# Kernel tuning notes

Hardware: AMD Instinct MI355X
Metric: run time of the kernel (lower is better)

## Reference

```python
import jax, jax.numpy as jnp
import numpy as np

B, L, DM = 2, 2048, 2048
H, P, N = 32, 64, 64          # n_heads, d_head, d_state
D_INNER = H * P               # 2048
PROJ = 2 * D_INNER + 2 * H * N + H  # 8224
EPS = 1e-5


def setup_inputs() -> dict:
    key = jax.random.key(0)
    k0, k1, k2 = jax.random.split(key, 3)
    return {
        "x": jax.random.normal(k0, (B, L, DM), jnp.float32),
        "W_in": jax.random.normal(k1, (PROJ, DM), jnp.float32) * (DM ** -0.5),
        "W_out": jax.random.normal(k2, (DM, D_INNER), jnp.float32) * (D_INNER ** -0.5),
        "gamma": jnp.ones((D_INNER,), jnp.float32),
        "beta": jnp.zeros((D_INNER,), jnp.float32),
        "D": jnp.ones((H, P), jnp.float32),
    }


def reference(x, W_in, W_out, gamma, beta, D):
    Bz, Lz, _ = x.shape
    zxbca = x @ W_in.T  # [B, L, PROJ]
    x_t, z_t, b_t, c_t, a_log = jnp.split(
        zxbca, [D_INNER, 2 * D_INNER, 2 * D_INNER + H * N, 2 * D_INNER + 2 * H * N], axis=-1)
    x_t = x_t.reshape(Bz, Lz, H, P)
    b_t = b_t.reshape(Bz, Lz, H, N)
    c_t = c_t.reshape(Bz, Lz, H, N)
    decay = jnp.exp(-jnp.exp(a_log))  # [B, L, H]

    def step(states, inp):
        # states: [B, H, P, N]
        xt, bt, ct, dec = inp  # [B,H,P], [B,H,N], [B,H,N], [B,H]
        states = states * dec[:, :, None, None] + xt[..., None] * bt[:, :, None, :]
        yt = jnp.einsum('bhpn,bhn->bhp', states, ct) + xt * D
        return states, yt

    init = jnp.zeros((Bz, H, P, N), x.dtype)
    xs = (jnp.moveaxis(x_t, 1, 0), jnp.moveaxis(b_t, 1, 0),
          jnp.moveaxis(c_t, 1, 0), jnp.moveaxis(decay, 1, 0))
    _, ys = jax.lax.scan(step, init, xs)  # ys: [L, B, H, P]
    y = jnp.moveaxis(ys, 0, 1).reshape(Bz, Lz, D_INNER)
    y = y * jax.nn.silu(z_t)
    mu = y.mean(-1, keepdims=True)
    var = y.var(-1, keepdims=True)
    y = (y - mu) * jax.lax.rsqrt(var + EPS) * gamma + beta
    return y @ W_out.T
```

## Files before the change

### kernel.cpp

```cpp
#include <hip/hip_runtime.h>
#include <stdint.h>
#include <stddef.h>

#define LSEQ   2048
#define DMODEL 2048
#define NH     32
#define DINNER 2048
#define PROJ   8224
#define PROJP  8192
#define NC     16
#define CHUNK  128

typedef __attribute__((ext_vector_type(4))) float f32x4;
typedef __attribute__((ext_vector_type(8))) __bf16 bf16x8;
typedef __attribute__((ext_vector_type(8))) unsigned short u16x8;

__device__ __forceinline__ unsigned short f2bf(float f) {
  union { float f; unsigned u; } uu; uu.f = f;
  unsigned r = uu.u + 0x7FFFu + ((uu.u >> 16) & 1u);
  return (unsigned short)(r >> 16);
}
__device__ __forceinline__ float bf2f(unsigned short u) {
  union { unsigned u; float f; } x; x.u = ((unsigned)u) << 16; return x.f;
}

__device__ __forceinline__ void gl_lds16(const void* g, void* l) {
  __builtin_amdgcn_global_load_lds(
      (__attribute__((address_space(1))) const void*)g,
      (__attribute__((address_space(3))) void*)l, 16, 0, 0);
}

__global__ __launch_bounds__(256) void cvt_f32_bf16(
    const float* __restrict__ in, unsigned short* __restrict__ out, int n) {
  int i = (blockIdx.x * 256 + threadIdx.x) * 4;
  if (i + 3 < n) {
    f32x4 v = *(const f32x4*)(in + i);
    ushort4 o;
    o.x = f2bf(v[0]); o.y = f2bf(v[1]); o.z = f2bf(v[2]); o.w = f2bf(v[3]);
    *(ushort4*)(out + i) = o;
  }
}

__global__ __launch_bounds__(512, 2) void gemm256(
    const unsigned short* __restrict__ A,
    const unsigned short* __restrict__ W,
    unsigned short* __restrict__ C, const int K, const int ldc, const int ntx) {
  __shared__ uint8_t sA[2][32768];
  __shared__ uint8_t sB[2][32768];
  const int tid  = threadIdx.x;
  const int lane = tid & 63;
  const int wid  = tid >> 6;
  const int wm   = wid >> 2;
  const int wnn  = wid & 3;
  const int nwg = gridDim.x;
  const int wg0 = blockIdx.x;
  const int g   = (wg0 & 7) * (nwg >> 3) + (wg0 >> 3);
  const int grp = ntx * 4;
  const int sr  = g / grp, rem = g % grp;
  const int m0  = (sr * 4 + (rem & 3)) * 256;
  const int n0  = (rem >> 2) * 256;

  const int row0 = wid * 8 + (lane >> 3);
  const int ssrc = (lane & 7) ^ (row0 & 7);
  const unsigned short* a_base = A + (size_t)(m0 + row0) * K + ssrc * 8;
  const unsigned short* b_base = W + (size_t)(n0 + row0) * K + ssrc * 8;
  const int wb = wid * 1024;

  f32x4 acc[8][4] = {};
  const int nk = K >> 6;

#pragma unroll
  for (int j = 0; j < 4; ++j) {
    gl_lds16(a_base + (size_t)j * 64 * K, &sA[0][j * 8192 + wb]);
    gl_lds16(b_base + (size_t)j * 64 * K, &sB[0][j * 8192 + wb]);
  }
  asm volatile("s_waitcnt vmcnt(0)" ::: "memory");
  asm volatile("s_barrier" ::: "memory");

  const int ra = wm * 128 + (lane & 15);
  const int rb = wnn * 64 + (lane & 15);
  const int hq = lane >> 4;

  for (int kt = 0; kt < nk; ++kt) {
    const int cur = kt & 1;
    const int nxt = cur ^ 1;
    const unsigned short* an = a_base + (size_t)(kt + 1) * 64;
    const unsigned short* wn_ = b_base + (size_t)(kt + 1) * 64;
    bf16x8 af[8], bv01[2], bv23[2];

    {
      const int s = hq;
#pragma unroll
      for (int mi = 0; mi < 8; ++mi) {
        const int r = ra + mi * 16;
        af[mi] = *(const bf16x8*)(&sA[cur][r * 128 + ((s ^ (r & 7)) << 4)]);
      }
#pragma unroll
      for (int ni = 0; ni < 2; ++ni) {
        const int r = rb + ni * 16;
        bv01[ni] = *(const bf16x8*)(&sB[cur][r * 128 + ((s ^ (r & 7)) << 4)]);
      }
    }
    asm volatile("s_barrier" ::: "memory");
    asm volatile("s_waitcnt lgkmcnt(0)" ::: "memory");
    if (kt + 1 < nk) {
      gl_lds16(an, &sA[nxt][wb]);
      gl_lds16(an + (size_t)64 * K, &sA[nxt][8192 + wb]);
      gl_lds16(wn_, &sB[nxt][wb]);
      gl_lds16(wn_ + (size_t)64 * K, &sB[nxt][8192 + wb]);
    }
    __builtin_amdgcn_s_setprio(1);
#pragma unroll
    for (int mi = 0; mi < 8; ++mi)
#pragma unroll
      for (int ni = 0; ni < 2; ++ni)
        acc[mi][ni] = __builtin_amdgcn_mfma_f32_16x16x32_bf16(
            af[mi], bv01[ni], acc[mi][ni], 0, 0, 0);
    __builtin_amdgcn_s_setprio(0);

    {
      const int s = hq;
#pragma unroll
      for (int ni = 0; ni < 2; ++ni) {
        const int r = rb + (ni + 2) * 16;
        bv23[ni] = *(const bf16x8*)(&sB[cur][r * 128 + ((s ^ (r & 7)) << 4)]);
      }
    }
    asm volatile("s_barrier" ::: "memory");
    asm volatile("s_waitcnt lgkmcnt(0)" ::: "memory");
    if (kt + 1 < nk) {
      gl_lds16(an + (size_t)128 * K, &sA[nxt][2 * 8192 + wb]);
      gl_lds16(an + (size_t)192 * K, &sA[nxt][3 * 8192 + wb]);
      gl_lds16(wn_ + (size_t)128 * K, &sB[nxt][2 * 8192 + wb]);
      gl_lds16(wn_ + (size_t)192 * K, &sB[nxt][3 * 8192 + wb]);
    }
    __builtin_amdgcn_s_setprio(1);
#pragma unroll
    for (int mi = 0; mi < 8; ++mi)
#pragma unroll
      for (int ni = 0; ni < 2; ++ni)
        acc[mi][ni + 2] = __builtin_amdgcn_mfma_f32_16x16x32_bf16(
            af[mi], bv23[ni], acc[mi][ni + 2], 0, 0, 0);
    __builtin_amdgcn_s_setprio(0);

    {
      const int s = 4 + hq;
#pragma unroll
      for (int mi = 0; mi < 8; ++mi) {
        const int r = ra + mi * 16;
        af[mi] = *(const bf16x8*)(&sA[cur][r * 128 + ((s ^ (r & 7)) << 4)]);
      }
#pragma unroll
      for (int ni = 0; ni < 2; ++ni) {
        const int r = rb + ni * 16;
        bv01[ni] = *(const bf16x8*)(&sB[cur][r * 128 + ((s ^ (r & 7)) << 4)]);
      }
    }
    asm volatile("s_barrier" ::: "memory");
    asm volatile("s_waitcnt lgkmcnt(0)" ::: "memory");
    __builtin_amdgcn_s_setprio(1);
#pragma unroll
    for (int mi = 0; mi < 8; ++mi)
#pragma unroll
      for (int ni = 0; ni < 2; ++ni)
        acc[mi][ni] = __builtin_amdgcn_mfma_f32_16x16x32_bf16(
            af[mi], bv01[ni], acc[mi][ni], 0, 0, 0);
    __builtin_amdgcn_s_setprio(0);

    {
      const int s = 4 + hq;
#pragma unroll
      for (int ni = 0; ni < 2; ++ni) {
        const int r = rb + (ni + 2) * 16;
        bv23[ni] = *(const bf16x8*)(&sB[cur][r * 128 + ((s ^ (r & 7)) << 4)]);
      }
    }
    asm volatile("s_waitcnt vmcnt(0)" ::: "memory");
    asm volatile("s_barrier" ::: "memory");
    asm volatile("s_waitcnt lgkmcnt(0)" ::: "memory");
    __builtin_amdgcn_s_setprio(1);
#pragma unroll
    for (int mi = 0; mi < 8; ++mi)
#pragma unroll
      for (int ni = 0; ni < 2; ++ni)
        acc[mi][ni + 2] = __builtin_amdgcn_mfma_f32_16x16x32_bf16(
            af[mi], bv23[ni], acc[mi][ni + 2], 0, 0, 0);
    __builtin_amdgcn_s_setprio(0);
  }

  const int crow = m0 + wm * 128 + (lane >> 4) * 4;
  const int ccol = n0 + wnn * 64 + (lane & 15);
#pragma unroll
  for (int mi = 0; mi < 8; ++mi)
#pragma unroll
    for (int ni = 0; ni < 4; ++ni) {
      unsigned short* cp = C + (size_t)(crow + mi * 16) * ldc + ccol + ni * 16;
      cp[0] = f2bf(acc[mi][ni][0]);
      cp[(size_t)ldc] = f2bf(acc[mi][ni][1]);
      cp[2 * (size_t)ldc] = f2bf(acc[mi][ni][2]);
      cp[3 * (size_t)ldc] = f2bf(acc[mi][ni][3]);
    }
}

__global__ __launch_bounds__(256) void gemm_bt(
    const unsigned short* __restrict__ A,
    const unsigned short* __restrict__ W,
    float* __restrict__ C, const int K, const int ldc, const int ntx) {
  __shared__ uint8_t sA[2][128 * 64 * 2];
  __shared__ uint8_t sB[2][128 * 64 * 2];
  const int tid  = threadIdx.x;
  const int lane = tid & 63;
  const int wid  = tid >> 6;
  const int wm   = wid >> 1;
  const int wnn  = wid & 1;
  const int nwg = gridDim.x;
  const int wg0 = blockIdx.x;
  const int g   = (wg0 & 7) * (nwg >> 3) + (wg0 >> 3);
  const int grp = ntx * 4;
  const int sr  = g / grp, rem = g % grp;
  const int m0  = (sr * 4 + (rem & 3)) * 128;
  const int n0  = (rem >> 2) * 128;

  const int rowA = tid >> 3;
  const int slot = (tid & 7) ^ (rowA & 7);
  const unsigned short* a_base = A + (size_t)(m0 + rowA) * K + slot * 8;
  const unsigned short* b_base = W + (size_t)(n0 + rowA) * K + slot * 8;
  const int loff = wid * 1024;

  f32x4 acc[4][4] = {};
  const int nk = K >> 6;

#pragma unroll
  for (int j = 0; j < 4; ++j) {
    gl_lds16(a_base + (size_t)j * 32 * K, &sA[0][loff + j * 4096]);
    gl_lds16(b_base + (size_t)j * 32 * K, &sB[0][loff + j * 4096]);
  }

  for (int kt = 0; kt < nk; ++kt) {
    const int cur = kt & 1;
    asm volatile("s_waitcnt vmcnt(0)" ::: "memory");
    asm volatile("s_barrier" ::: "memory");
    if (kt + 1 < nk) {
      const unsigned short* ak = a_base + (kt + 1) * 64;
      const unsigned short* bk = b_base + (kt + 1) * 64;
      const int nb = cur ^ 1;
#pragma unroll
      for (int j = 0; j < 4; ++j) {
        gl_lds16(ak + (size_t)j * 32 * K, &sA[nb][loff + j * 4096]);
        gl_lds16(bk + (size_t)j * 32 * K, &sB[nb][loff + j * 4096]);
      }
    }

    const int ra = wm * 64 + (lane & 15);
    const int rb = wnn * 64 + (lane & 15);
    const int hq = lane >> 4;
#pragma unroll
    for (int ks = 0; ks < 2; ++ks) {
      bf16x8 af[4], bv[4];
      const int s = ks * 4 + hq;
#pragma unroll
      for (int mi = 0; mi < 4; ++mi) {
        const int r = ra + mi * 16;
        af[mi] = *(const bf16x8*)(&sA[cur][r * 128 + ((s ^ (r & 7)) << 4)]);
      }
#pragma unroll
      for (int ni = 0; ni < 4; ++ni) {
        const int r = rb + ni * 16;
        bv[ni] = *(const bf16x8*)(&sB[cur][r * 128 + ((s ^ (r & 7)) << 4)]);
      }
#pragma unroll
      for (int mi = 0; mi < 4; ++mi)
#pragma unroll
        for (int ni = 0; ni < 4; ++ni)
          acc[mi][ni] = __builtin_amdgcn_mfma_f32_16x16x32_bf16(
              af[mi], bv[ni], acc[mi][ni], 0, 0, 0);
    }
  }

  const int crow = m0 + wm * 64 + (lane >> 4) * 4;
  const int ccol = n0 + wnn * 64 + (lane & 15);
#pragma unroll
  for (int mi = 0; mi < 4; ++mi)
#pragma unroll
    for (int ni = 0; ni < 4; ++ni) {
      float* cp = C + (size_t)(crow + mi * 16) * ldc + ccol + ni * 16;
      cp[0] = acc[mi][ni][0];
      cp[(size_t)ldc] = acc[mi][ni][1];
      cp[2 * (size_t)ldc] = acc[mi][ni][2];
      cp[3 * (size_t)ldc] = acc[mi][ni][3];
    }
}

#define AR  64
#define AKT 128
__global__ __launch_bounds__(256) void alog_part(
    const float* __restrict__ x, const float* __restrict__ W_in,
    float* __restrict__ P) {
  __shared__ float sX[AR][132];
  __shared__ float sW[32][132];
  const int tid = threadIdx.x;
  const int row0 = blockIdx.x * AR;
  const int k0 = blockIdx.y * 256;
  const int r = tid >> 2;
  const int oq = (tid & 3) * 8;
  float acc[8] = {};
#pragma unroll
  for (int kt = 0; kt < 256; kt += AKT) {
    __syncthreads();
    {
      const int lr = tid >> 2;
      const int kk = (tid & 3) * 32;
      const float* src = x + (size_t)(row0 + lr) * DMODEL + k0 + kt + kk;
      float* dst = &sX[lr][kk];
#pragma unroll
      for (int j = 0; j < 32; j += 4)
        *(f32x4*)(dst + j) = *(const f32x4*)(src + j);
    }
    {
      const int wr = tid >> 3;
      const int kk = (tid & 7) * 16;
      const float* src = W_in + (size_t)(8192 + wr) * DMODEL + k0 + kt + kk;
      float* dst = &sW[wr][kk];
#pragma unroll
      for (int j = 0; j < 16; j += 4)
        *(f32x4*)(dst + j) = *(const f32x4*)(src + j);
    }
    __syncthreads();
#pragma unroll 2
    for (int k = 0; k < AKT; k += 4) {
      f32x4 xv = *(const f32x4*)&sX[r][k];
#pragma unroll
      for (int o = 0; o < 8; ++o) {
        f32x4 wv = *(const f32x4*)&sW[oq + o][k];
        acc[o] = fmaf(xv[0], wv[0], acc[o]);
        acc[o] = fmaf(xv[1], wv[1], acc[o]);
        acc[o] = fmaf(xv[2], wv[2], acc[o]);
        acc[o] = fmaf(xv[3], wv[3], acc[o]);
      }
    }
  }
  float* dst = P + ((size_t)blockIdx.y * 4096 + row0 + r) * 32 + oq;
  f32x4 v0 = {acc[0], acc[1], acc[2], acc[3]};
  f32x4 v1 = {acc[4], acc[5], acc[6], acc[7]};
  *(f32x4*)dst = v0; *(f32x4*)(dst + 4) = v1;
}

__global__ __launch_bounds__(256) void alog_reduce(
    const float* __restrict__ P, float* __restrict__ Alog) {
  const int idx = blockIdx.x * 256 + threadIdx.x;
  const int row = idx >> 5, o = idx & 31;
  float s = 0.f;
#pragma unroll
  for (int c = 0; c < 8; ++c) s += P[((size_t)c * 4096 + row) * 32 + o];
  Alog[(size_t)row * 32 + o] = s;
}

__global__ __launch_bounds__(256) void mm_pass1(
    const unsigned short* __restrict__ zx, const float* __restrict__ Alog,
    float* __restrict__ Sfin, float* __restrict__ Dprod) {
  __shared__ uint8_t sXw[16384];
  __shared__ uint8_t sBT[16384];
  __shared__ float logd[128];
  __shared__ float cums[128];
  const int tid = threadIdx.x;
  const int chunk = blockIdx.x;
  const int bh = blockIdx.y;
  const int h = bh & 31, b = bh >> 5;
  const size_t bL0 = (size_t)b * LSEQ + (size_t)chunk * CHUNK;

  if (tid < 128) logd[tid] = -__expf(Alog[(bL0 + tid) * 32 + h]);
  __syncthreads();
  if (tid < 128) {
    float s = 0.f;
#pragma unroll 4
    for (int r = 0; r <= tid; ++r) s += logd[r];
    cums[tid] = s;
  }
  __syncthreads();
  const float clast = cums[127];

  {
    const int u = tid & 127, ph = (tid >> 7) * 32;
    const int half = u >> 6, uk = u & 63;
    const float wfac = __expf(clast - cums[u]);
    const unsigned short* xrow = zx + (bL0 + u) * (size_t)PROJP + h * 64 + ph;
#pragma unroll
    for (int j = 0; j < 4; ++j) {
      u16x8 xv = *(const u16x8*)(xrow + j * 8);
      u16x8 bv = *(const u16x8*)(xrow + 4096 + j * 8);
#pragma unroll
      for (int e = 0; e < 8; ++e) {
        const int p = ph + j * 8 + e;
        const int byteoff = half * 8192 + p * 128 +
                            (((uk >> 3) ^ (p & 7)) << 4) + (uk & 7) * 2;
        *(unsigned short*)(sXw + byteoff) = f2bf(bf2f(xv[e]) * wfac);
        *(unsigned short*)(sBT + byteoff) = bv[e];
      }
    }
  }
  __syncthreads();

  const int lane = tid & 63, w = tid >> 6;
  const int ra = w * 16 + (lane & 15);
  const int s0 = lane >> 4;
  f32x4 acc[4] = {};
#pragma unroll
  for (int half = 0; half < 2; ++half)
#pragma unroll
    for (int ks = 0; ks < 2; ++ks) {
      const int s = ks * 4 + s0;
      bf16x8 af = *(const bf16x8*)(sXw + half * 8192 + ra * 128 + ((s ^ (ra & 7)) << 4));
#pragma unroll
      for (int ni = 0; ni < 4; ++ni) {
        const int rb = ni * 16 + (lane & 15);
        bf16x8 bf = *(const bf16x8*)(sBT + half * 8192 + rb * 128 + ((s ^ (rb & 7)) << 4));
        acc[ni] = __builtin_amdgcn_mfma_f32_16x16x32_bf16(af, bf, acc[ni], 0, 0, 0);
      }
    }

  float* sf = Sfin + ((size_t)bh * NC + chunk) * 4096;
  const int prow = w * 16 + (lane >> 4) * 4;
  const int ncol = lane & 15;
#pragma unroll
  for (int ni = 0; ni < 4; ++ni)
#pragma unroll
    for (int reg = 0; reg < 4; ++reg)
      sf[(size_t)(prow + reg) * 64 + ni * 16 + ncol] = acc[ni][reg];
  if (tid == 0) Dprod[bh * NC + chunk] = __expf(clast);
}

__global__ __launch_bounds__(256) void scan_combine(
    const float* __restrict__ Sfin, const float* __restrict__ Dp,
    float* __restrict__ Sini) {
  const int idx = blockIdx.x * 256 + threadIdx.x;
  const int bh = idx >> 12;
  const int e = idx & 4095;
  const float* sf = Sfin + (size_t)bh * NC * 4096 + e;
  float* si = Sini + (size_t)bh * NC * 4096 + e;
  float S = 0.f;
#pragma unroll
  for (int c = 0; c < NC; ++c) {
    si[(size_t)c * 4096] = S;
    if (c < NC - 1) S = fmaf(S, Dp[bh * NC + c], sf[(size_t)c * 4096]);
  }
}

__global__ __launch_bounds__(256) void mm_pass2(
    const unsigned short* __restrict__ zx, const float* __restrict__ Alog,
    const float* __restrict__ Sini, float* __restrict__ y) {
  __shared__ uint8_t smem[65536];
  __shared__ float logd[128];
  __shared__ float cums[128];
  const int tid = threadIdx.x;
  const int chunk = blockIdx.x;
  const int bh = blockIdx.y;
  const int h = bh & 31, b = bh >> 5;
  const size_t bL0 = (size_t)b * LSEQ + (size_t)chunk * CHUNK;
  const int lane = tid & 63, w = tid >> 6;

  if (tid < 128) logd[tid] = -__expf(Alog[(bL0 + tid) * 32 + h]);
  {
    const int rowS = tid >> 3;
    const int slot = (tid & 7) ^ (rowS & 7);
    const unsigned short* cb = zx + (bL0 + rowS) * (size_t)PROJP + 6144 + h * 64 + slot * 8;
    const unsigned short* bb = zx + (bL0 + rowS) * (size_t)PROJP + 4096 + h * 64 + slot * 8;
    const int dbase = w * 1024;
#pragma unroll
    for (int j = 0; j < 4; ++j) {
      gl_lds16(cb + (size_t)j * 32 * PROJP, smem + dbase + j * 4096);
      gl_lds16(bb + (size_t)j * 32 * PROJP, smem + 16384 + dbase + j * 4096);
    }
  }
  __syncthreads();
  if (tid < 128) {
    float s = 0.f;
#pragma unroll 4
    for (int r = 0; r <= tid; ++r) s += logd[r];
    cums[tid] = s;
  }
  {
    const int u = tid & 127, ph = (tid >> 7) * 32;
    const int half = u >> 6, uk = u & 63;
    const unsigned short* xrow = zx + (bL0 + u) * (size_t)PROJP + h * 64 + ph;
#pragma unroll
    for (int j = 0; j < 4; ++j) {
      u16x8 xv = *(const u16x8*)(xrow + j * 8);
#pragma unroll
      for (int e = 0; e < 8; ++e) {
        const int p = ph + j * 8 + e;
        *(unsigned short*)(smem + 32768 + half * 8192 + p * 128 +
                           (((uk >> 3) ^ (p & 7)) << 4) + (uk & 7) * 2) = xv[e];
      }
    }
  }
  {
    const float* si = Sini + ((size_t)bh * NC + chunk) * 4096 + tid * 16;
    const int p = tid >> 2;
#pragma unroll
    for (int gq = 0; gq < 2; ++gq) {
      u16x8 hv, lv;
#pragma unroll
      for (int e = 0; e < 8; ++e) {
        float v = si[gq * 8 + e];
        unsigned short hu = f2bf(v);
        hv[e] = hu;
        lv[e] = f2bf(v - bf2f(hu));
      }
      const int slotg = (tid & 3) * 2 + gq;
      const int byte_ = p * 128 + ((slotg ^ (p & 7)) << 4);
      *(u16x8*)(smem + 49152 + byte_) = hv;
      *(u16x8*)(smem + 57344 + byte_) = lv;
    }
  }
  __syncthreads();

  const int rl = lane & 15, s0 = lane >> 4;
  const int tb = w * 32;
  f32x4 accG[2][8] = {};
  f32x4 acc2[2][4] = {};
#pragma unroll
  for (int ks = 0; ks < 2; ++ks) {
    const int s = ks * 4 + s0;
    bf16x8 ca[2];
#pragma unroll
    for (int mi = 0; mi < 2; ++mi) {
      const int r = tb + mi * 16 + rl;
      ca[mi] = *(const bf16x8*)(smem + r * 128 + ((s ^ (r & 7)) << 4));
    }
#pragma unroll
    for (int ni = 0; ni < 8; ++ni) {
      const int r = ni * 16 + rl;
      bf16x8 bf = *(const bf16x8*)(smem + 16384 + r * 128 + ((s ^ (r & 7)) << 4));
#pragma unroll
      for (int mi = 0; mi < 2; ++mi)
        accG[mi][ni] = __builtin_amdgcn_mfma_f32_16x16x32_bf16(ca[mi], bf, accG[mi][ni], 0, 0, 0);
    }
#pragma unroll
    for (int ni = 0; ni < 4; ++ni) {
      const int r = ni * 16 + rl;
      bf16x8 sh = *(const bf16x8*)(smem + 49152 + r * 128 + ((s ^ (r & 7)) << 4));
      bf16x8 sl = *(const bf16x8*)(smem + 57344 + r * 128 + ((s ^ (r & 7)) << 4));
#pragma unroll
      for (int mi = 0; mi < 2; ++mi) {
        acc2[mi][ni] = __builtin_amdgcn_mfma_f32_16x16x32_bf16(ca[mi], sh, acc2[mi][ni], 0, 0, 0);
        acc2[mi][ni] = __builtin_amdgcn_mfma_f32_16x16x32_bf16(ca[mi], sl, acc2[mi][ni], 0, 0, 0);
      }
    }
  }
  __syncthreads();

  float ct[2][4];
#pragma unroll
  for (int mi = 0; mi < 2; ++mi)
#pragma unroll
    for (int reg = 0; reg < 4; ++reg)
      ct[mi][reg] = cums[tb + mi * 16 + (lane >> 4) * 4 + reg];
#pragma unroll
  for (int ni = 0; ni < 8; ++ni) {
    const int u = ni * 16 + rl;
    const float cu = cums[u];
    const int Ph = u >> 6, uk = u & 63;
#pragma unroll
    for (int mi = 0; mi < 2; ++mi)
#pragma unroll
      for (int reg = 0; reg < 4; ++reg) {
        const int t = tb + mi * 16 + (lane >> 4) * 4 + reg;
        float v = (u <= t) ? accG[mi][ni][reg] * __expf(ct[mi][reg] - cu) : 0.f;
        *(unsigned short*)(smem + Ph * 16384 + t * 128 +
                           (((uk >> 3) ^ (t & 7)) << 4) + (uk & 7) * 2) = f2bf(v);
      }
  }
  __syncthreads();

  f32x4 accY[2][4] = {};
#pragma unroll
  for (int half = 0; half < 2; ++half)
#pragma unroll
    for (int ks = 0; ks < 2; ++ks) {
      const int s = ks * 4 + s0;
      bf16x8 pa[2];
#pragma unroll
      for (int mi = 0; mi < 2; ++mi) {
        const int r = tb + mi * 16 + rl;
        pa[mi] = *(const bf16x8*)(smem + half * 16384 + r * 128 + ((s ^ (r & 7)) << 4));
      }
#pragma unroll
      for (int ni = 0; ni < 4; ++ni) {
        const int r = ni * 16 + rl;
        bf16x8 xb = *(const bf16x8*)(smem + 32768 + half * 8192 + r * 128 + ((s ^ (r & 7)) << 4));
#pragma unroll
        for (int mi = 0; mi < 2; ++mi)
          accY[mi][ni] = __builtin_amdgcn_mfma_f32_16x16x32_bf16(pa[mi], xb, accY[mi][ni], 0, 0, 0);
      }
    }

#pragma unroll
  for (int mi = 0; mi < 2; ++mi)
#pragma unroll
    for (int reg = 0; reg < 4; ++reg) {
      const int t = tb + mi * 16 + (lane >> 4) * 4 + reg;
      const float wt = __expf(ct[mi][reg]);
#pragma unroll
      for (int ni = 0; ni < 4; ++ni) {
        const int p = ni * 16 + rl;
        y[(bL0 + t) * (size_t)DINNER + h * 64 + p] =
            accY[mi][ni][reg] + wt * acc2[mi][ni][reg];
      }
    }
}

__global__ __launch_bounds__(256) void siluln(
    const float* __restrict__ yin, const unsigned short* __restrict__ zx,
    const float* __restrict__ Dmat,
    const float* __restrict__ gamma, const float* __restrict__ beta,
    unsigned short* __restrict__ out) {
  const int row = blockIdx.x;
  const int tid = threadIdx.x;
  const int lane = tid & 63;
  const int wid = tid >> 6;
  const int col = tid * 8;
  const float* yp = yin + (size_t)row * DINNER + col;
  const unsigned short* zp = zx + (size_t)row * PROJP + DINNER + col;
  const unsigned short* xp = zx + (size_t)row * PROJP + col;
  f32x4 y0 = *(const f32x4*)yp, y1 = *(const f32x4*)(yp + 4);
  u16x8 zv = *(const u16x8*)zp;
  u16x8 xv = *(const u16x8*)xp;
  f32x4 d0 = *(const f32x4*)(Dmat + col), d1 = *(const f32x4*)(Dmat + col + 4);
  float v[8];
#pragma unroll
  for (int i = 0; i < 8; ++i) {
    float z = bf2f(zv[i]);
    float dd = (i < 4) ? d0[i] : d1[i - 4];
    float yy = ((i < 4) ? y0[i] : y1[i - 4]) + bf2f(xv[i]) * dd;
    v[i] = yy * (z / (1.f + __expf(-z)));
  }
  float t1 = 0.f, t2 = 0.f;
#pragma unroll
  for (int i = 0; i < 8; ++i) { t1 += v[i]; t2 += v[i] * v[i]; }
#pragma unroll
  for (int off = 1; off < 64; off <<= 1) {
    t1 += __shfl_xor(t1, off);
    t2 += __shfl_xor(t2, off);
  }
  __shared__ float red[8];
  if (lane == 0) { red[wid] = t1; red[wid + 4] = t2; }
  __syncthreads();
  float ts1 = red[0] + red[1] + red[2] + red[3];
  float ts2 = red[4] + red[5] + red[6] + red[7];
  float mu = ts1 * (1.f / 2048.f);
  float var = ts2 * (1.f / 2048.f) - mu * mu;
  float rs = rsqrtf(var + 1e-5f);
  f32x4 g0 = *(const f32x4*)(gamma + col), g1 = *(const f32x4*)(gamma + col + 4);
  f32x4 b0 = *(const f32x4*)(beta + col),  b1 = *(const f32x4*)(beta + col + 4);
  u16x8 ov;
#pragma unroll
  for (int i = 0; i < 4; ++i)
    ov[i] = f2bf((v[i] - mu) * rs * g0[i] + b0[i]);
#pragma unroll
  for (int i = 0; i < 4; ++i)
    ov[i + 4] = f2bf((v[i + 4] - mu) * rs * g1[i] + b1[i]);
  *(u16x8*)(out + (size_t)row * DINNER + col) = ov;
}

extern "C" void kernel_launch(void* const* d_in, const int* in_sizes, int n_in,
                              void* d_out, int out_size, void* d_ws, size_t ws_size,
                              hipStream_t stream) {
  (void)in_sizes; (void)n_in; (void)out_size; (void)ws_size;
  const float* x     = (const float*)d_in[0];
  const float* W_in  = (const float*)d_in[1];
  const float* W_out = (const float*)d_in[2];
  const float* gamma = (const float*)d_in[3];
  const float* beta  = (const float*)d_in[4];
  const float* Dmat  = (const float*)d_in[5];

  uint8_t* ws = (uint8_t*)d_ws;
  unsigned short* xbf = (unsigned short*)ws;
  unsigned short* wbf = (unsigned short*)(ws + 16777216);
  float* Palog = (float*)(ws + 16777216);
  float* Sfin  = (float*)(ws + 16777216);
  float* Sini  = (float*)(ws + 33554432);
  float* Dprod = (float*)(ws + 50331648);
  float* Alog  = (float*)(ws + 50855936);
  unsigned short* zxb = (unsigned short*)(ws + 51380224);
  float* ybuf = (float*)(ws + 119537664);

  cvt_f32_bf16<<<8192, 256, 0, stream>>>(x, xbf, 8388608);
  cvt_f32_bf16<<<16384, 256, 0, stream>>>(W_in, wbf, 16777216);
  gemm256<<<512, 512, 0, stream>>>(xbf, wbf, zxb, 2048, PROJP, 32);
  alog_part<<<dim3(64, 8), 256, 0, stream>>>(x, W_in, Palog);
  alog_reduce<<<512, 256, 0, stream>>>(Palog, Alog);
  mm_pass1<<<dim3(NC - 1, 64), 256, 0, stream>>>(zxb, Alog, Sfin, Dprod);
  scan_combine<<<1024, 256, 0, stream>>>(Sfin, Dprod, Sini);
  mm_pass2<<<dim3(NC, 64), 256, 0, stream>>>(zxb, Alog, Sini, ybuf);
  siluln<<<4096, 256, 0, stream>>>(ybuf, zxb, Dmat, gamma, beta, xbf);
  cvt_f32_bf16<<<4096, 256, 0, stream>>>(W_out, wbf, 4194304);
  gemm_bt<<<512, 256, 0, stream>>>(xbf, wbf, (float*)d_out, 2048, 2048, 16);
}
```

Before: 302.6 us.

## Restructure gemm256 into quadrant phases with staggered async prefetch

```diff
diff --git a/kernel.cpp b/kernel.cpp
--- a/kernel.cpp
+++ b/kernel.cpp
@@ -50,8 +50,8 @@
   const int tid  = threadIdx.x;
   const int lane = tid & 63;
   const int wid  = tid >> 6;
-  const int wm   = wid >> 2;
-  const int wnn  = wid & 3;
+  const int iw   = wid & 3;
+  const int jw   = wid >> 2;
   const int nwg = gridDim.x;
   const int wg0 = blockIdx.x;
   const int g   = (wg0 & 7) * (nwg >> 3) + (wg0 >> 3);
@@ -66,140 +66,110 @@
   const unsigned short* b_base = W + (size_t)(n0 + row0) * K + ssrc * 8;
   const int wb = wid * 1024;
 
-  f32x4 acc[8][4] = {};
+  f32x4 acc[2][2][2][4] = {};
   const int nk = K >> 6;
-
-#pragma unroll
-  for (int j = 0; j < 4; ++j) {
-    gl_lds16(a_base + (size_t)j * 64 * K, &sA[0][j * 8192 + wb]);
-    gl_lds16(b_base + (size_t)j * 64 * K, &sB[0][j * 8192 + wb]);
-  }
+  const int rl = lane & 15;
+  const int hq = lane >> 4;
+
+  gl_lds16(a_base, &sA[0][wb]);
+  gl_lds16(a_base + (size_t)64 * K, &sA[0][8192 + wb]);
+  gl_lds16(b_base, &sB[0][wb]);
+  gl_lds16(b_base + (size_t)64 * K, &sB[0][8192 + wb]);
+  gl_lds16(b_base + (size_t)128 * K, &sB[0][2 * 8192 + wb]);
+  gl_lds16(b_base + (size_t)192 * K, &sB[0][3 * 8192 + wb]);
+  gl_lds16(a_base + (size_t)128 * K, &sA[0][2 * 8192 + wb]);
+  gl_lds16(a_base + (size_t)192 * K, &sA[0][3 * 8192 + wb]);
   asm volatile("s_waitcnt vmcnt(0)" ::: "memory");
   asm volatile("s_barrier" ::: "memory");
 
-  const int ra = wm * 128 + (lane & 15);
-  const int rb = wnn * 64 + (lane & 15);
-  const int hq = lane >> 4;
+#define PHASE(MH, NH)                                                         \
+  {                                                                           \
+    bf16x8 af[2][2], bv[2][4];                                                \
+    _Pragma("unroll")                                                         \
+    for (int ks = 0; ks < 2; ++ks) {                                          \
+      const int s = ks * 4 + hq;                                              \
+      _Pragma("unroll")                                                       \
+      for (int mi = 0; mi < 2; ++mi) {                                        \
+        const int r = (MH)*128 + iw * 32 + mi * 16 + rl;                      \
+        af[ks][mi] = *(const bf16x8*)(&sA[cur][r * 128 + ((s ^ (r & 7)) << 4)]); \
+      }                                                                       \
+      _Pragma("unroll")                                                       \
+      for (int ni = 0; ni < 4; ++ni) {                                        \
+        const int r = (NH)*128 + jw * 64 + ni * 16 + rl;                      \
+        bv[ks][ni] = *(const bf16x8*)(&sB[cur][r * 128 + ((s ^ (r & 7)) << 4)]); \
+      }                                                                       \
+    }                                                                         \
+    asm volatile("s_waitcnt lgkmcnt(0)" ::: "memory");                        \
+    __builtin_amdgcn_s_setprio(1);                                            \
+    _Pragma("unroll")                                                         \
+    for (int ks = 0; ks < 2; ++ks)                                            \
+      _Pragma("unroll")                                                       \
+      for (int mi = 0; mi < 2; ++mi)                                          \
+        _Pragma("unroll")                                                     \
+        for (int ni = 0; ni < 4; ++ni)                                        \
+          acc[MH][mi][NH][ni] = __builtin_amdgcn_mfma_f32_16x16x32_bf16(      \
+              af[ks][mi], bv[ks][ni], acc[MH][mi][NH][ni], 0, 0, 0);          \
+    __builtin_amdgcn_s_setprio(0);                                            \
+  }
 
   for (int kt = 0; kt < nk; ++kt) {
     const int cur = kt & 1;
-    const int nxt = cur ^ 1;
+    const int nb = cur ^ 1;
     const unsigned short* an = a_base + (size_t)(kt + 1) * 64;
-    const unsigned short* wn_ = b_base + (size_t)(kt + 1) * 64;
-    bf16x8 af[8], bv01[2], bv23[2];
-
-    {
-      const int s = hq;
-#pragma unroll
-      for (int mi = 0; mi < 8; ++mi) {
-        const int r = ra + mi * 16;
-        af[mi] = *(const bf16x8*)(&sA[cur][r * 128 + ((s ^ (r & 7)) << 4)]);
-      }
-#pragma unroll
-      for (int ni = 0; ni < 2; ++ni) {
-        const int r = rb + ni * 16;
-        bv01[ni] = *(const bf16x8*)(&sB[cur][r * 128 + ((s ^ (r & 7)) << 4)]);
-      }
-    }
+    const unsigned short* bn = b_base + (size_t)(kt + 1) * 64;
+    const bool more = (kt + 1 < nk);
+
+    asm volatile("s_waitcnt vmcnt(4)" ::: "memory");
     asm volatile("s_barrier" ::: "memory");
-    asm volatile("s_waitcnt lgkmcnt(0)" ::: "memory");
-    if (kt + 1 < nk) {
-      gl_lds16(an, &sA[nxt][wb]);
-      gl_lds16(an + (size_t)64 * K, &sA[nxt][8192 + wb]);
-      gl_lds16(wn_, &sB[nxt][wb]);
-      gl_lds16(wn_ + (size_t)64 * K, &sB[nxt][8192 + wb]);
-    }
-    __builtin_amdgcn_s_setprio(1);
-#pragma unroll
-    for (int mi = 0; mi < 8; ++mi)
-#pragma unroll
-      for (int ni = 0; ni < 2; ++ni)
-        acc[mi][ni] = __builtin_amdgcn_mfma_f32_16x16x32_bf16(
-            af[mi], bv01[ni], acc[mi][ni], 0, 0, 0);
-    __builtin_amdgcn_s_setprio(0);
-
-    {
-      const int s = hq;
-#pragma unroll
-      for (int ni = 0; ni < 2; ++ni) {
-        const int r = rb + (ni + 2) * 16;
-        bv23[ni] = *(const bf16x8*)(&sB[cur][r * 128 + ((s ^ (r & 7)) << 4)]);
-      }
-    }
+    if (more) {
+      gl_lds16(an, &sA[nb][wb]);
+      gl_lds16(an + (size_t)64 * K, &sA[nb][8192 + wb]);
+    }
+    PHASE(0, 0)
+
+    if (more) { asm volatile("s_waitcnt vmcnt(4)" ::: "memory"); }
+    else      { asm volatile("s_waitcnt vmcnt(2)" ::: "memory"); }
     asm volatile("s_barrier" ::: "memory");
-    asm volatile("s_waitcnt lgkmcnt(0)" ::: "memory");
-    if (kt + 1 < nk) {
-      gl_lds16(an + (size_t)128 * K, &sA[nxt][2 * 8192 + wb]);
-      gl_lds16(an + (size_t)192 * K, &sA[nxt][3 * 8192 + wb]);
-      gl_lds16(wn_ + (size_t)128 * K, &sB[nxt][2 * 8192 + wb]);
-      gl_lds16(wn_ + (size_t)192 * K, &sB[nxt][3 * 8192 + wb]);
-    }
-    __builtin_amdgcn_s_setprio(1);
-#pragma unroll
-    for (int mi = 0; mi < 8; ++mi)
-#pragma unroll
-      for (int ni = 0; ni < 2; ++ni)
-        acc[mi][ni + 2] = __builtin_amdgcn_mfma_f32_16x16x32_bf16(
-            af[mi], bv23[ni], acc[mi][ni + 2], 0, 0, 0);
-    __builtin_amdgcn_s_setprio(0);
-
-    {
-      const int s = 4 + hq;
-#pragma unroll
-      for (int mi = 0; mi < 8; ++mi) {
-        const int r = ra + mi * 16;
-        af[mi] = *(const bf16x8*)(&sA[cur][r * 128 + ((s ^ (r & 7)) << 4)]);
-      }
-#pragma unroll
-      for (int ni = 0; ni < 2; ++ni) {
-        const int r = rb + ni * 16;
-        bv01[ni] = *(const bf16x8*)(&sB[cur][r * 128 + ((s ^ (r & 7)) << 4)]);
-      }
-    }
+    if (more) {
+      gl_lds16(bn, &sB[nb][wb]);
+      gl_lds16(bn + (size_t)64 * K, &sB[nb][8192 + wb]);
+    }
+    PHASE(0, 1)
+
+    if (more) { asm volatile("s_waitcnt vmcnt(4)" ::: "memory"); }
+    else      { asm volatile("s_waitcnt vmcnt(0)" ::: "memory"); }
     asm volatile("s_barrier" ::: "memory");
-    asm volatile("s_waitcnt lgkmcnt(0)" ::: "memory");
-    __builtin_amdgcn_s_setprio(1);
-#pragma unroll
-    for (int mi = 0; mi < 8; ++mi)
-#pragma unroll
-      for (int ni = 0; ni < 2; ++ni)
-        acc[mi][ni] = __builtin_amdgcn_mfma_f32_16x16x32_bf16(
-            af[mi], bv01[ni], acc[mi][ni], 0, 0, 0);
-    __builtin_amdgcn_s_setprio(0);
-
-    {
-      const int s = 4 + hq;
-#pragma unroll
-      for (int ni = 0; ni < 2; ++ni) {
-        const int r = rb + (ni + 2) * 16;
-        bv23[ni] = *(const bf16x8*)(&sB[cur][r * 128 + ((s ^ (r & 7)) << 4)]);
-      }
-    }
-    asm volatile("s_waitcnt vmcnt(0)" ::: "memory");
+    if (more) {
+      gl_lds16(bn + (size_t)128 * K, &sB[nb][2 * 8192 + wb]);
+      gl_lds16(bn + (size_t)192 * K, &sB[nb][3 * 8192 + wb]);
+    }
+    PHASE(1, 0)
+
     asm volatile("s_barrier" ::: "memory");
-    asm volatile("s_waitcnt lgkmcnt(0)" ::: "memory");
-    __builtin_amdgcn_s_setprio(1);
-#pragma unroll
-    for (int mi = 0; mi < 8; ++mi)
-#pragma unroll
-      for (int ni = 0; ni < 2; ++ni)
-        acc[mi][ni + 2] = __builtin_amdgcn_mfma_f32_16x16x32_bf16(
-            af[mi], bv23[ni], acc[mi][ni + 2], 0, 0, 0);
-    __builtin_amdgcn_s_setprio(0);
-  }
-
-  const int crow = m0 + wm * 128 + (lane >> 4) * 4;
-  const int ccol = n0 + wnn * 64 + (lane & 15);
-#pragma unroll
-  for (int mi = 0; mi < 8; ++mi)
-#pragma unroll
-    for (int ni = 0; ni < 4; ++ni) {
-      unsigned short* cp = C + (size_t)(crow + mi * 16) * ldc + ccol + ni * 16;
-      cp[0] = f2bf(acc[mi][ni][0]);
-      cp[(size_t)ldc] = f2bf(acc[mi][ni][1]);
-      cp[2 * (size_t)ldc] = f2bf(acc[mi][ni][2]);
-      cp[3 * (size_t)ldc] = f2bf(acc[mi][ni][3]);
-    }
+    if (more) {
+      gl_lds16(an + (size_t)128 * K, &sA[nb][2 * 8192 + wb]);
+      gl_lds16(an + (size_t)192 * K, &sA[nb][3 * 8192 + wb]);
+    }
+    PHASE(1, 1)
+  }
+#undef PHASE
+
+#pragma unroll
+  for (int mh = 0; mh < 2; ++mh)
+#pragma unroll
+    for (int mi = 0; mi < 2; ++mi)
+#pragma unroll
+      for (int nh = 0; nh < 2; ++nh)
+#pragma unroll
+        for (int ni = 0; ni < 4; ++ni) {
+          const int crow = m0 + mh * 128 + iw * 32 + mi * 16 + (lane >> 4) * 4;
+          const int ccol = n0 + nh * 128 + jw * 64 + ni * 16 + rl;
+          unsigned short* cp = C + (size_t)crow * ldc + ccol;
+          cp[0] = f2bf(acc[mh][mi][nh][ni][0]);
+          cp[(size_t)ldc] = f2bf(acc[mh][mi][nh][ni][1]);
+          cp[2 * (size_t)ldc] = f2bf(acc[mh][mi][nh][ni][2]);
+          cp[3 * (size_t)ldc] = f2bf(acc[mh][mi][nh][ni][3]);
+        }
 }
 
 __global__ __launch_bounds__(256) void gemm_bt(
```

New measurement: 371.2 us. +22.7%, slower.
